# Kernel tuning notes

Hardware: AMD Instinct MI355X
Metric: run time of the kernel (lower is better)

## Reference

```python
import jax, jax.numpy as jnp
import numpy as np

B_, T_, N_ = 32, 96, 68
IN_F, HID, GRU_H, NCLS = 3, 128, 128, 10
DEG = 8
N_NODES = B_ * T_ * N_
N_EDGES = N_NODES * DEG


def setup_inputs() -> dict:
    key = jax.random.key(0)
    ks = jax.random.split(key, 16)
    s = 0.05
    rn = lambda k, shp: (jax.random.normal(k, shp, jnp.float32) * s)
    return {
        "x": jax.random.normal(ks[0], (N_NODES, IN_F), jnp.float32),
        "edge_index": jax.random.randint(ks[1], (2, N_EDGES), 0, N_NODES, jnp.int32),
        "W_gcn0": rn(ks[2], (IN_F, HID)),
        "b_gcn0": jnp.zeros((HID,), jnp.float32),
        "W_gcn1": rn(ks[3], (HID, HID)),
        "b_gcn1": jnp.zeros((HID,), jnp.float32),
        "W_mlp": rn(ks[4], (HID, HID)),
        "b_mlp": jnp.zeros((HID,), jnp.float32),
        "W_ih": rn(ks[5], (3 * GRU_H, HID)),
        "W_hh": rn(ks[6], (3 * GRU_H, GRU_H)),
        "b_ih": jnp.zeros((3 * GRU_H,), jnp.float32),
        "b_hh": jnp.zeros((3 * GRU_H,), jnp.float32),
        "W_c1": rn(ks[7], (GRU_H, GRU_H // 2)),
        "b_c1": jnp.zeros((GRU_H // 2,), jnp.float32),
        "W_c2": rn(ks[8], (GRU_H // 2, NCLS)),
        "b_c2": jnp.zeros((NCLS,), jnp.float32),
        "B": B_, "T": T_, "N": N_,
    }


def reference(x, edge_index, W_gcn0, b_gcn0, W_gcn1, b_gcn1, W_mlp, b_mlp,
              W_ih, W_hh, b_ih, b_hh, W_c1, b_c1, W_c2, b_c2, B, T, N):
    n_nodes = x.shape[0]
    src, dst = edge_index[0], edge_index[1]
    # GCN degree with self-loops: deg[i] = 1 + in-degree(i)
    deg = jnp.ones((n_nodes,), x.dtype).at[dst].add(1.0)
    d_isqrt = jax.lax.rsqrt(deg)
    self_norm = (d_isqrt * d_isqrt)[:, None]  # self-loop norm = 1/deg
    edge_norm = (d_isqrt[src] * d_isqrt[dst])[:, None]

    def gcn(h, W, b):
        h = h @ W
        agg = jax.ops.segment_sum(h[src] * edge_norm, dst, num_segments=n_nodes)
        return agg + h * self_norm + b

    h = jax.nn.relu(gcn(x, W_gcn0, b_gcn0))
    h = jax.nn.relu(gcn(h, W_gcn1, b_gcn1))
    h = jax.nn.relu(h @ W_mlp + b_mlp)  # node_mlp (dropout off in eval)

    frames = h.reshape(B, T, N, -1).mean(axis=2)  # [B, T, HID] frame pooling

    def gru_step(hs, xt):
        gi = xt @ W_ih.T + b_ih
        gh = hs @ W_hh.T + b_hh
        ir, iz, inn = jnp.split(gi, 3, axis=-1)
        hr, hz, hn = jnp.split(gh, 3, axis=-1)
        r = jax.nn.sigmoid(ir + hr)
        z = jax.nn.sigmoid(iz + hz)
        n_new = jnp.tanh(inn + r * hn)
        return (1.0 - z) * n_new + z * hs, None

    h0 = jnp.zeros((B, GRU_H), frames.dtype)
    hT, _ = jax.lax.scan(gru_step, h0, jnp.swapaxes(frames, 0, 1))

    hidden = jax.nn.relu(hT @ W_c1 + b_c1)
    return hidden @ W_c2 + b_c2  # logits [B, num_classes]
```

## Files before the change

### kernel.cpp

```cpp
#include <hip/hip_runtime.h>

#define NN_TOT 208896
#define E_TOT  1671168
#define B_SZ   32
#define T_SZ   96
#define NPF    68
#define HID    128
#define NBINS  204
#define CAP    9216
#define NSB    816

typedef _Float16 f16x8 __attribute__((ext_vector_type(8)));
typedef _Float16 f16x2v __attribute__((ext_vector_type(2)));
typedef float f32x4 __attribute__((ext_vector_type(4)));

__global__ __launch_bounds__(256) void k_scatter(const int* __restrict__ src, const int* __restrict__ dst,
                                                 int* __restrict__ gcur, int* __restrict__ er_tmp,
                                                 const float* __restrict__ Wih, const float* __restrict__ Whh,
                                                 const float* __restrict__ W1, const float* __restrict__ Wm,
                                                 const float* __restrict__ W0, const float* __restrict__ b0,
                                                 _Float16* __restrict__ Wihh, _Float16* __restrict__ Wihl,
                                                 _Float16* __restrict__ W1p, _Float16* __restrict__ Wmp,
                                                 _Float16* __restrict__ Whhp, _Float16* __restrict__ W0h,
                                                 _Float16* __restrict__ b0h) {
    const int bid = blockIdx.x;
    const int tid = threadIdx.x;
    if (bid >= NSB) {
        int i = (bid - NSB) * 256 + tid;
        {
            int e = i & 7;
            int lane = (i >> 3) & 63;
            int f = i >> 9;
            int j = f >> 2, kk = f & 3;
            int q = lane >> 4, p = lane & 15;
            float wv = Wih[(size_t)(j * 16 + p) * 128 + kk * 32 + q * 8 + e];
            _Float16 hi = (_Float16)wv;
            Wihh[i] = hi;
            Wihl[i] = (_Float16)(wv - (float)hi);
        }
        {
            int e = i & 7;
            int lane = (i >> 3) & 63;
            int f = i >> 9;
            int kk = f & 3, g = (f >> 2) % 3, wv = f / 12;
            int q = lane >> 4, c = lane & 15;
            Whhp[i] = (_Float16)Whh[(size_t)(g * 128 + 16 * wv + c) * 128 + kk * 32 + q * 8 + e];
        }
        if (i < 16384) {
            int f = i >> 9;
            int j = f >> 2, kk = f & 3;
            int lane = (i >> 3) & 63;
            int e = i & 7;
            int q = lane >> 4, p = lane & 15;
            int k = kk * 32 + q * 8 + e, n = j * 16 + p;
            W1p[i] = (_Float16)W1[k * 128 + n];
            Wmp[i] = (_Float16)Wm[k * 128 + n];
        }
        if (i < 384) W0h[i] = (_Float16)W0[i];
        if (i < 128) b0h[i] = (_Float16)b0[i];
        return;
    }
    __shared__ int hist[NBINS];
    __shared__ int lofs[NBINS];
    __shared__ int lbase[NBINS];
    __shared__ int ts[256];
    __shared__ int recs[2048];
    __shared__ int dsta[2048];
    for (int i = tid; i < NBINS; i += 256) hist[i] = 0;
    __syncthreads();
    const int be = bid * 2048 + tid * 8;
    int s[8], d[8], rk[8];
    *(int4*)&s[0] = *(const int4*)&src[be];
    *(int4*)&s[4] = *(const int4*)&src[be + 4];
    *(int4*)&d[0] = *(const int4*)&dst[be];
    *(int4*)&d[4] = *(const int4*)&dst[be + 4];
#pragma unroll
    for (int j = 0; j < 8; ++j) rk[j] = atomicAdd(&hist[d[j] >> 10], 1);
    __syncthreads();
    {
        int v = (tid < NBINS) ? hist[tid] : 0;
        ts[tid] = v;
        __syncthreads();
        int inc = v;
        for (int off = 1; off < 256; off <<= 1) {
            int add = (tid >= off) ? ts[tid - off] : 0;
            __syncthreads();
            inc += add;
            ts[tid] = inc;
            __syncthreads();
        }
        if (tid < NBINS) lofs[tid] = inc - v;
    }
    for (int i = tid; i < NBINS; i += 256) lbase[i] = atomicAdd(&gcur[i], hist[i]);
    __syncthreads();
#pragma unroll
    for (int j = 0; j < 8; ++j) {
        int b = d[j] >> 10;
        int pos = lofs[b] + rk[j];
        recs[pos] = s[j] | ((d[j] & 1023) << 18);
        dsta[pos] = b * CAP + lbase[b] + rk[j];
    }
    __syncthreads();
#pragma unroll
    for (int it = 0; it < 8; ++it) {
        int p = tid + it * 256;
        er_tmp[dsta[p]] = recs[p];
    }
}

__global__ __launch_bounds__(256) void k_binsort2(const int* __restrict__ er_tmp, const int* __restrict__ gcur,
                                                  const float* __restrict__ x, int* __restrict__ er,
                                                  int2* __restrict__ row2, float4* __restrict__ xd) {
    __shared__ int lcnt[1024];
    __shared__ int lofs[1024];
    __shared__ int ts[256];
    const int tid = threadIdx.x;
    const int nb = blockIdx.x << 10;
    const int base0 = blockIdx.x * CAP;
    for (int i = tid; i < 1024; i += 256) lcnt[i] = 0;
    __syncthreads();
    const int nrec = gcur[blockIdx.x];
    int rec[36];
#pragma unroll
    for (int j = 0; j < 36; ++j) {
        int idx = tid + j * 256;
        rec[j] = (idx < nrec) ? er_tmp[base0 + idx] : -1;
    }
#pragma unroll
    for (int j = 0; j < 36; ++j)
        if (rec[j] >= 0) atomicAdd(&lcnt[rec[j] >> 18], 1);
    __syncthreads();
    const int base = tid * 4;
    const int c0 = lcnt[base], c1 = lcnt[base + 1], c2 = lcnt[base + 2], c3 = lcnt[base + 3];
    int ssum = c0 + c1 + c2 + c3;
    ts[tid] = ssum;
    __syncthreads();
    int inc = ssum;
    for (int off = 1; off < 256; off <<= 1) {
        int add = (tid >= off) ? ts[tid - off] : 0;
        __syncthreads();
        inc += add;
        ts[tid] = inc;
        __syncthreads();
    }
    const int b0 = base0 + (inc - ssum);
    lofs[base] = b0;
    lofs[base + 1] = b0 + c0;
    lofs[base + 2] = b0 + c0 + c1;
    lofs[base + 3] = b0 + c0 + c1 + c2;
    row2[nb + base] = make_int2(b0, b0 + c0);
    row2[nb + base + 1] = make_int2(b0 + c0, b0 + c0 + c1);
    row2[nb + base + 2] = make_int2(b0 + c0 + c1, b0 + c0 + c1 + c2);
    row2[nb + base + 3] = make_int2(b0 + c0 + c1 + c2, b0 + ssum);
    {
        const float4* xv = (const float4*)(x + 3 * (size_t)(nb + base));
        float4 a = xv[0], b = xv[1], c = xv[2];
        float i0 = 1.0f / sqrtf(1.f + (float)c0);
        float i1 = 1.0f / sqrtf(1.f + (float)c1);
        float i2 = 1.0f / sqrtf(1.f + (float)c2);
        float i3 = 1.0f / sqrtf(1.f + (float)c3);
        xd[nb + base + 0] = make_float4(a.x * i0, a.y * i0, a.z * i0, i0);
        xd[nb + base + 1] = make_float4(a.w * i1, b.x * i1, b.y * i1, i1);
        xd[nb + base + 2] = make_float4(b.z * i2, b.w * i2, c.x * i2, i2);
        xd[nb + base + 3] = make_float4(c.y * i3, c.z * i3, c.w * i3, i3);
    }
    __syncthreads();
#pragma unroll
    for (int j = 0; j < 36; ++j)
        if (rec[j] >= 0) {
            int p = atomicAdd(&lofs[rec[j] >> 18], 1);
            er[p] = rec[j] & 0x3FFFF;
        }
}

__global__ __launch_bounds__(256) void k_z0(const float4* __restrict__ xd, const int2* __restrict__ row2,
                                            const int* __restrict__ er, float4* __restrict__ z0out) {
    const int tid = threadIdx.x;
    const int blk = blockIdx.x;
    const int li = tid >> 2;
    const int slot = tid & 3;
    const int n = blk * 64 + li;
    const int2 be2 = row2[n];
    float p0 = 0.f, p1 = 0.f, p2 = 0.f;
    for (int ei = be2.x + slot; ei < be2.y; ei += 4) {
        float4 f = xd[er[ei]];
        p0 += f.x;
        p1 += f.y;
        p2 += f.z;
    }
    p0 += __shfl_xor(p0, 1); p1 += __shfl_xor(p1, 1); p2 += __shfl_xor(p2, 1);
    p0 += __shfl_xor(p0, 2); p1 += __shfl_xor(p1, 2); p2 += __shfl_xor(p2, 2);
    if (slot == 0) {
        const float4 own = xd[n];
        const float w = own.w;
        float4 z;
        z.x = w * (p0 + own.x);
        z.y = w * (p1 + own.y);
        z.z = w * (p2 + own.z);
        z.w = w;
        z0out[n] = z;
    }
}

__global__ __launch_bounds__(256, 4) void k_agg_mm(const float4* __restrict__ z0, const int2* __restrict__ row2,
                                                   const int* __restrict__ er, const _Float16* __restrict__ W0h,
                                                   const _Float16* __restrict__ b0h, const _Float16* __restrict__ W1p,
                                                   const float* __restrict__ b1, const _Float16* __restrict__ Wmp,
                                                   const float* __restrict__ bm, float* __restrict__ fr32, int bofs) {
    __shared__ __align__(16) _Float16 As[64 * 136];
    __shared__ __align__(16) _Float16 Bs[64 * 136];
    __shared__ float colpart[4 * 2 * 128];
    const int tid = threadIdx.x;
    const int w = tid >> 6, lane = tid & 63;
    const int blk = blockIdx.x + bofs;

    {
        const int node = blk * 64 + lane;
        const int2 be2 = row2[node];
        const int beg = be2.x, end = be2.y;
        int ei = beg;
        int sa_c = 0, sb_c = 0, sa_n = 0, sb_n = 0;
        float4 za_c, zb_c;
        if (ei + 2 <= end) { sa_c = er[ei]; sb_c = er[ei + 1]; }
        if (ei + 4 <= end) { sa_n = er[ei + 2]; sb_n = er[ei + 3]; }
        const float4 zs = z0[node];
        if (ei + 2 <= end) { za_c = z0[sa_c]; zb_c = z0[sb_c]; }

        const f16x2v* __restrict__ W0p = (const f16x2v*)W0h;
        const f16x2v* __restrict__ b0p = (const f16x2v*)b0h;
        const int pb = w * 16;
        const f16x2v zero2 = {(_Float16)0.f, (_Float16)0.f};
        f16x2v w0p[16], w1p[16], w2p[16], bbp[16];
#pragma unroll
        for (int j = 0; j < 16; ++j) {
            w0p[j] = W0p[pb + j];
            w1p[j] = W0p[64 + pb + j];
            w2p[j] = W0p[128 + pb + j];
            bbp[j] = b0p[pb + j];
        }
        const _Float16 isd = (_Float16)zs.w;
        const f16x2v dnn = {isd, isd};
        f16x2v accp[16];
        {
            _Float16 sx = (_Float16)zs.x, sy = (_Float16)zs.y, sz = (_Float16)zs.z;
            f16x2v zxx = {sx, sx}, zyy = {sy, sy}, zzz = {sz, sz};
#pragma unroll
            for (int j = 0; j < 16; ++j) {
                f16x2v t = zxx * w0p[j] + (zyy * w1p[j] + (zzz * w2p[j] + bbp[j]));
                t = __builtin_elementwise_max(t, zero2);
                accp[j] = t * dnn;
            }
        }
        for (; ei + 2 <= end; ei += 2) {
            float4 za_nv, zb_nv;
            int sa_nn = 0, sb_nn = 0;
            if (ei + 4 <= end) { za_nv = z0[sa_n]; zb_nv = z0[sb_n]; }
            if (ei + 6 <= end) { sa_nn = er[ei + 4]; sb_nn = er[ei + 5]; }
            const float4 za = za_c, zb = zb_c;
            _Float16 ax = (_Float16)za.x, ay = (_Float16)za.y, az = (_Float16)za.z;
            _Float16 aen = (_Float16)za.w;
            _Float16 bx = (_Float16)zb.x, by = (_Float16)zb.y, bz = (_Float16)zb.z;
            _Float16 ben = (_Float16)zb.w;
            f16x2v axx = {ax, ax}, ayy = {ay, ay}, azz = {az, az}, aee = {aen, aen};
            f16x2v bxx = {bx, bx}, byy = {by, by}, bzz = {bz, bz}, bee = {ben, ben};
#pragma unroll
            for (int j = 0; j < 16; ++j) {
                f16x2v t = axx * w0p[j] + (ayy * w1p[j] + (azz * w2p[j] + bbp[j]));
                t = __builtin_elementwise_max(t, zero2);
                accp[j] = t * aee + accp[j];
            }
#pragma unroll
            for (int j = 0; j < 16; ++j) {
                f16x2v t = bxx * w0p[j] + (byy * w1p[j] + (bzz * w2p[j] + bbp[j]));
                t = __builtin_elementwise_max(t, zero2);
                accp[j] = t * bee + accp[j];
            }
            za_c = za_nv; zb_c = zb_nv;
            sa_n = sa_nn; sb_n = sb_nn;
        }
        if (ei < end) {
            float4 za = z0[er[ei]];
            _Float16 ax = (_Float16)za.x, ay = (_Float16)za.y, az = (_Float16)za.z;
            _Float16 aen = (_Float16)za.w;
            f16x2v axx = {ax, ax}, ayy = {ay, ay}, azz = {az, az}, aee = {aen, aen};
#pragma unroll
            for (int j = 0; j < 16; ++j) {
                f16x2v t = axx * w0p[j] + (ayy * w1p[j] + (azz * w2p[j] + bbp[j]));
                t = __builtin_elementwise_max(t, zero2);
                accp[j] = t * aee + accp[j];
            }
        }
        _Float16* dst = &As[lane * 136 + w * 32];
#pragma unroll
        for (int j = 0; j < 16; ++j) *(f16x2v*)(dst + 2 * j) = accp[j] * dnn;
    }
    __syncthreads();

    const int q = lane >> 4, c = lane & 15;
    {
        f16x8 afr[4];
#pragma unroll
        for (int kk = 0; kk < 4; ++kk) afr[kk] = *(const f16x8*)(&As[(w * 16 + c) * 136 + kk * 32 + q * 8]);
        const f16x8* __restrict__ Bv = (const f16x8*)W1p;
#pragma unroll
        for (int j = 0; j < 8; ++j) {
            f32x4 cc = {0.f, 0.f, 0.f, 0.f};
#pragma unroll
            for (int kk = 0; kk < 4; ++kk)
                cc = __builtin_amdgcn_mfma_f32_16x16x32_f16(afr[kk], Bv[(j * 4 + kk) * 64 + lane], cc, 0, 0, 0);
            const float bi = b1[j * 16 + c];
#pragma unroll
            for (int r = 0; r < 4; ++r)
                Bs[(w * 16 + q * 4 + r) * 136 + j * 16 + c] = (_Float16)fmaxf(cc[r] + bi, 0.f);
        }
    }

    {
        f16x8 afr2[4];
#pragma unroll
        for (int kk = 0; kk < 4; ++kk) afr2[kk] = *(const f16x8*)(&Bs[(w * 16 + c) * 136 + kk * 32 + q * 8]);
        const f16x8* __restrict__ Bv2 = (const f16x8*)Wmp;
        const int f0 = (blk * 64) / NPF;
        const int cut = (f0 + 1) * NPF;
        const int rowg0 = blk * 64 + w * 16 + q * 4;
#pragma unroll
        for (int j = 0; j < 8; ++j) {
            f32x4 cc = {0.f, 0.f, 0.f, 0.f};
#pragma unroll
            for (int kk = 0; kk < 4; ++kk)
                cc = __builtin_amdgcn_mfma_f32_16x16x32_f16(afr2[kk], Bv2[(j * 4 + kk) * 64 + lane], cc, 0, 0, 0);
            const float bi = bm[j * 16 + c];
            float sA = 0.f, sB = 0.f;
#pragma unroll
            for (int r = 0; r < 4; ++r) {
                float v = fmaxf(cc[r] + bi, 0.f);
                if (rowg0 + r < cut) sA += v; else sB += v;
            }
            sA += __shfl_xor(sA, 16);
            sA += __shfl_xor(sA, 32);
            sB += __shfl_xor(sB, 16);
            sB += __shfl_xor(sB, 32);
            if (lane < 16) {
                colpart[(w * 2 + 0) * 128 + j * 16 + c] = sA;
                colpart[(w * 2 + 1) * 128 + j * 16 + c] = sB;
            }
        }
    }
    __syncthreads();
    {
        const int f = tid >> 7, col = tid & 127;
        float s = colpart[(0 * 2 + f) * 128 + col] + colpart[(1 * 2 + f) * 128 + col] +
                  colpart[(2 * 2 + f) * 128 + col] + colpart[(3 * 2 + f) * 128 + col];
        const int f0 = (blk * 64) / NPF;
        if (f == 0) {
            atomicAdd(&fr32[(size_t)f0 * 128 + col], s);
        } else {
            const int f1 = (blk * 64 + 63) / NPF;
            if (f1 != f0) atomicAdd(&fr32[(size_t)f1 * 128 + col], s);
        }
    }
}

__global__ __launch_bounds__(256) void k_gi(const float* __restrict__ fr32,
                                            const _Float16* __restrict__ Wihh, const _Float16* __restrict__ Wihl,
                                            const float* __restrict__ bih, const float* __restrict__ bhh,
                                            float* __restrict__ GIt) {
    __shared__ __align__(16) _Float16 Ah[64 * 136];
    __shared__ __align__(16) _Float16 Al[64 * 136];
    const int tid = threadIdx.x;
    const int w = tid >> 6, lane = tid & 63;
    const int q = lane >> 4, p = lane & 15;
    const int nb = blockIdx.x * 64;

    for (int idx = tid; idx < 64 * 128; idx += 256) {
        int row = idx >> 7, col = idx & 127;
        float v = fr32[(size_t)(nb + row) * 128 + col] * (1.0f / NPF);
        _Float16 hi = (_Float16)v;
        Ah[row * 136 + col] = hi;
        Al[row * 136 + col] = (_Float16)(v - (float)hi);
    }
    __syncthreads();

    f16x8 ah[4], al[4];
#pragma unroll
    for (int kk = 0; kk < 4; ++kk) {
        ah[kk] = *(const f16x8*)(&Ah[(w * 16 + p) * 136 + kk * 32 + q * 8]);
        al[kk] = *(const f16x8*)(&Al[(w * 16 + p) * 136 + kk * 32 + q * 8]);
    }
    const f16x8* __restrict__ Bh = (const f16x8*)Wihh;
    const f16x8* __restrict__ Bl = (const f16x8*)Wihl;
    int dr[4];
#pragma unroll
    for (int r = 0; r < 4; ++r) {
        int m = nb + w * 16 + q * 4 + r;
        int bb = m / 96, tt = m - bb * 96;
        dr[r] = (tt * B_SZ + bb) * 384;
    }
#pragma unroll
    for (int j = 0; j < 24; ++j) {
        f32x4 cc = {0.f, 0.f, 0.f, 0.f};
#pragma unroll
        for (int kk = 0; kk < 4; ++kk)
            cc = __builtin_amdgcn_mfma_f32_16x16x32_f16(ah[kk], Bh[(j * 4 + kk) * 64 + lane], cc, 0, 0, 0);
#pragma unroll
        for (int kk = 0; kk < 4; ++kk)
            cc = __builtin_amdgcn_mfma_f32_16x16x32_f16(ah[kk], Bl[(j * 4 + kk) * 64 + lane], cc, 0, 0, 0);
#pragma unroll
        for (int kk = 0; kk < 4; ++kk)
            cc = __builtin_amdgcn_mfma_f32_16x16x32_f16(al[kk], Bh[(j * 4 + kk) * 64 + lane], cc, 0, 0, 0);
        const int o = j * 16 + p;
        const float bias = bih[o] + ((o < 256) ? bhh[o] : 0.f);
        const float scale = (o < 256) ? -1.44269504f : 1.f;
#pragma unroll
        for (int r = 0; r < 4; ++r) GIt[dr[r] + o] = (cc[r] + bias) * scale;
    }
}

#define GRU_SYNC()                                              \
    asm volatile("s_waitcnt lgkmcnt(0)" ::: "memory");          \
    __builtin_amdgcn_s_barrier();                               \
    __builtin_amdgcn_sched_barrier(0);

#define GRU_BODY(PAR, GU, GL, JOFF)                                                                  \
    {                                                                                                \
        const _Float16* rb = hbuf[PAR];                                                              \
        _Float16* wb = hbuf[PAR ^ 1];                                                                \
        f16x8 afr[4];                                                                                \
        _Pragma("unroll") for (int kk = 0; kk < 4; ++kk)                                             \
            afr[kk] = *(const f16x8*)(&rb[c * 144 + kk * 32 + q * 8]);                               \
        const float* lp = pb + (size_t)(JOFF + 2) * STRIDE;                                          \
        _Pragma("unroll") for (int r = 0; r < 4; ++r)                                                \
            _Pragma("unroll") for (int g = 0; g < 3; ++g)                                            \
                GL[r * 3 + g] = lp[r * 384 + g * 128];                                               \
        f32x4 cc[3];                                                                                 \
        _Pragma("unroll") for (int g = 0; g < 3; ++g) {                                              \
            f32x4 a = {0.f, 0.f, 0.f, 0.f};                                                          \
            _Pragma("unroll") for (int kk = 0; kk < 4; ++kk)                                         \
                a = __builtin_amdgcn_mfma_f32_16x16x32_f16(afr[kk], bfr[g][kk], a, 0, 0, 0);         \
            cc[g] = a;                                                                               \
        }                                                                                            \
        _Pragma("unroll") for (int r = 0; r < 4; ++r) {                                              \
            float hn = cc[2][r] + bh2;                                                               \
            float rg = __builtin_amdgcn_rcpf(1.f + exp2f(fmaf(mL2E, cc[0][r], GU[r * 3 + 0])));      \
            float zg = __builtin_amdgcn_rcpf(1.f + exp2f(fmaf(mL2E, cc[1][r], GU[r * 3 + 1])));      \
            float arg = fmaf(rg, hn, GU[r * 3 + 2]);                                                 \
            float u = __builtin_amdgcn_rcpf(exp2f(2.f * L2E * arg) + 1.f);                           \
            float nn = fmaf(-2.f, u, 1.f);                                                           \
            h[r] = fmaf(zg, h[r] - nn, nn);                                                          \
            if (q < 2) wb[(q * 4 + r) * 144 + 16 * w + c] = (_Float16)h[r];                          \
        }                                                                                            \
        GRU_SYNC()                                                                                   \
    }

__global__ __launch_bounds__(512) __attribute__((amdgpu_waves_per_eu(1, 2)))
void k_gru(const float* __restrict__ GIt, const _Float16* __restrict__ Whhp,
           const float* __restrict__ bhh,
           const float* __restrict__ Wc1, const float* __restrict__ bc1,
           const float* __restrict__ Wc2, const float* __restrict__ bc2,
           float* __restrict__ out, float* __restrict__ hst,
           int t0, int iters, int last) {
    __shared__ __align__(16) _Float16 hbuf[2][16 * 144];
    const int tid = threadIdx.x;
    const int w = tid >> 6, lane = tid & 63;
    const int q = lane >> 4, c = lane & 15;
    const int B = blockIdx.x;
    const float L2E = 1.44269504f;
    const float mL2E = -1.44269504f;
    const int STRIDE = B_SZ * 384;

    f16x8 bfr[3][4];
#pragma unroll
    for (int g = 0; g < 3; ++g)
#pragma unroll
        for (int kk = 0; kk < 4; ++kk)
            bfr[g][kk] = *(const f16x8*)(Whhp + (size_t)(((w * 3 + g) * 4 + kk) * 64 + lane) * 8);
    const float bh2 = bhh[256 + 16 * w + c];
    for (int i = tid; i < 2 * 16 * 144 / 2; i += 512) ((unsigned int*)hbuf)[i] = 0u;
    float h[4] = {0.f, 0.f, 0.f, 0.f};

    const int qq = (q < 2) ? q : 1;
    if (t0 != 0) {
#pragma unroll
        for (int r = 0; r < 4; ++r) h[r] = hst[(size_t)(B * 8 + qq * 4 + r) * 128 + 16 * w + c];
    }
    const float* pb = GIt + (size_t)t0 * STRIDE + (size_t)(B * 8 + qq * 4) * 384 + 16 * w + c;
    float g0[12], g1[12], g2[12];
#pragma unroll
    for (int r = 0; r < 4; ++r)
#pragma unroll
        for (int g = 0; g < 3; ++g) {
            g0[r * 3 + g] = pb[r * 384 + g * 128];
            g1[r * 3 + g] = pb[STRIDE + r * 384 + g * 128];
        }
    __syncthreads();
    if (t0 != 0 && q < 2) {
#pragma unroll
        for (int r = 0; r < 4; ++r) hbuf[0][(q * 4 + r) * 144 + 16 * w + c] = (_Float16)h[r];
    }
    GRU_SYNC()

    for (int it = 0; it < iters; ++it) {
        GRU_BODY(0, g0, g2, 0)
        GRU_BODY(1, g1, g0, 1)
        GRU_BODY(0, g2, g1, 2)
        GRU_BODY(1, g0, g2, 3)
        GRU_BODY(0, g1, g0, 4)
        GRU_BODY(1, g2, g1, 5)
        pb += 6 * (size_t)STRIDE;
    }

    if (!last) {
        if (q < 2) {
#pragma unroll
            for (int r = 0; r < 4; ++r) hst[(size_t)(B * 8 + q * 4 + r) * 128 + 16 * w + c] = h[r];
        }
        return;
    }

    float* hbf = (float*)hbuf;
    float* hid = hbf + 1024;
    __syncthreads();
    if (q < 2) {
#pragma unroll
        for (int r = 0; r < 4; ++r) hbf[(q * 4 + r) * 128 + 16 * w + c] = h[r];
    }
    __syncthreads();
    {
        const int b = tid >> 6, j = tid & 63;
        const float* hb = hbf + b * 128;
        float a0 = bc1[j], a1 = 0.f, a2 = 0.f, a3 = 0.f;
#pragma unroll
        for (int k = 0; k < 128; k += 4) {
            a0 = fmaf(hb[k], Wc1[k * 64 + j], a0);
            a1 = fmaf(hb[k + 1], Wc1[(k + 1) * 64 + j], a1);
            a2 = fmaf(hb[k + 2], Wc1[(k + 2) * 64 + j], a2);
            a3 = fmaf(hb[k + 3], Wc1[(k + 3) * 64 + j], a3);
        }
        hid[tid] = fmaxf((a0 + a1) + (a2 + a3), 0.f);
    }
    __syncthreads();
    if (tid < 80) {
        int b = tid / 10, cc2 = tid % 10;
        float a = bc2[cc2];
#pragma unroll 8
        for (int k = 0; k < 64; ++k) a = fmaf(hid[b * 64 + k], Wc2[k * 10 + cc2], a);
        out[(B * 8 + b) * 10 + cc2] = a;
    }
}

extern "C" void kernel_launch(void* const* d_in, const int* in_sizes, int n_in, void* d_out, int out_size, void* d_ws,
                              size_t ws_size, hipStream_t stream) {
    const float* x = (const float*)d_in[0];
    const int* ei = (const int*)d_in[1];
    const int* e_src = ei;
    const int* e_dst = ei + E_TOT;
    const float* W0 = (const float*)d_in[2];
    const float* b0 = (const float*)d_in[3];
    const float* W1 = (const float*)d_in[4];
    const float* b1 = (const float*)d_in[5];
    const float* Wm = (const float*)d_in[6];
    const float* bm = (const float*)d_in[7];
    const float* Wih = (const float*)d_in[8];
    const float* Whh = (const float*)d_in[9];
    const float* bih = (const float*)d_in[10];
    const float* bhh = (const float*)d_in[11];
    const float* Wc1 = (const float*)d_in[12];
    const float* bc1 = (const float*)d_in[13];
    const float* Wc2 = (const float*)d_in[14];
    const float* bc2 = (const float*)d_in[15];
    float* out = (float*)d_out;

    char* base = (char*)d_ws;
    size_t off = 0;
    auto alloc = [&](size_t bytes) {
        size_t o = off;
        off = (off + bytes + 255) & ~(size_t)255;
        return o;
    };
    size_t o_gcur = alloc(256 * 4);
    size_t o_row2 = alloc((size_t)NN_TOT * 8);
    size_t o_er = alloc((size_t)NBINS * CAP * 4);
    size_t o_ertmp = alloc((size_t)NBINS * CAP * 4);
    size_t o_xd = alloc((size_t)NN_TOT * 16);
    size_t o_fr32 = alloc((size_t)B_SZ * T_SZ * 128 * 4);
    size_t o_gi = alloc((size_t)(T_SZ + 2) * B_SZ * 384 * 4);
    size_t o_hst = alloc((size_t)B_SZ * 128 * 4);
    size_t o_wihh = alloc((size_t)384 * 128 * 2);
    size_t o_wihl = alloc((size_t)384 * 128 * 2);
    size_t o_w1p = alloc((size_t)128 * 128 * 2);
    size_t o_wmp = alloc((size_t)128 * 128 * 2);
    size_t o_whhp = alloc((size_t)128 * 384 * 2);
    size_t o_w0h = alloc((size_t)384 * 2);
    size_t o_b0h = alloc((size_t)128 * 2);
    size_t o_z0 = alloc((size_t)NN_TOT * 16);
    if (off > ws_size) return;

    int* gcur = (int*)(base + o_gcur);
    int2* row2 = (int2*)(base + o_row2);
    int* er = (int*)(base + o_er);
    int* er_tmp = (int*)(base + o_ertmp);
    float4* xd = (float4*)(base + o_xd);
    float* fr32 = (float*)(base + o_fr32);
    float* GIt = (float*)(base + o_gi);
    float* hst = (float*)(base + o_hst);
    _Float16* Wihh = (_Float16*)(base + o_wihh);
    _Float16* Wihl = (_Float16*)(base + o_wihl);
    _Float16* W1p = (_Float16*)(base + o_w1p);
    _Float16* Wmp = (_Float16*)(base + o_wmp);
    _Float16* Whhp = (_Float16*)(base + o_whhp);
    _Float16* W0h = (_Float16*)(base + o_w0h);
    _Float16* b0h = (_Float16*)(base + o_b0h);
    float4* z0 = (float4*)(base + o_z0);

    hipMemsetAsync(base + o_gcur, 0, 256 * 4, stream);
    hipMemsetAsync(base + o_fr32, 0, (size_t)B_SZ * T_SZ * 128 * 4, stream);

    k_scatter<<<NSB + 192, 256, 0, stream>>>(e_src, e_dst, gcur, er_tmp,
                                             Wih, Whh, W1, Wm, W0, b0,
                                             Wihh, Wihl, W1p, Wmp, Whhp, W0h, b0h);
    k_binsort2<<<NBINS, 256, 0, stream>>>(er_tmp, gcur, x, er, row2, xd);
    k_z0<<<NN_TOT / 64, 256, 0, stream>>>(xd, row2, er, z0);
    k_agg_mm<<<1088, 256, 0, stream>>>(z0, row2, er, W0h, b0h, W1p, b1, Wmp, bm, fr32, 0);
    k_agg_mm<<<1088, 256, 0, stream>>>(z0, row2, er, W0h, b0h, W1p, b1, Wmp, bm, fr32, 1088);
    k_agg_mm<<<1088, 256, 0, stream>>>(z0, row2, er, W0h, b0h, W1p, b1, Wmp, bm, fr32, 2176);
    k_gi<<<B_SZ * T_SZ / 64, 256, 0, stream>>>(fr32, Wihh, Wihl, bih, bhh, GIt);
    k_gru<<<4, 512, 0, stream>>>(GIt, Whhp, bhh, Wc1, bc1, Wc2, bc2, out, hst, 0, 5, 0);
    k_gru<<<4, 512, 0, stream>>>(GIt, Whhp, bhh, Wc1, bc1, Wc2, bc2, out, hst, 30, 5, 0);
    k_gru<<<4, 512, 0, stream>>>(GIt, Whhp, bhh, Wc1, bc1, Wc2, bc2, out, hst, 60, 6, 1);
}
```

Measured before the change: 370.0 us.

## Merge split kernel launches, fold fr32 memset into scatter, precompute bin ranks

```diff
diff --git a/kernel.cpp b/kernel.cpp
--- a/kernel.cpp
+++ b/kernel.cpp
@@ -22,11 +22,16 @@
                                                  _Float16* __restrict__ Wihh, _Float16* __restrict__ Wihl,
                                                  _Float16* __restrict__ W1p, _Float16* __restrict__ Wmp,
                                                  _Float16* __restrict__ Whhp, _Float16* __restrict__ W0h,
-                                                 _Float16* __restrict__ b0h) {
+                                                 _Float16* __restrict__ b0h, float4* __restrict__ fr32v) {
     const int bid = blockIdx.x;
     const int tid = threadIdx.x;
     if (bid >= NSB) {
         int i = (bid - NSB) * 256 + tid;
+        {
+            const float4 z4 = make_float4(0.f, 0.f, 0.f, 0.f);
+            fr32v[(size_t)i * 2] = z4;
+            fr32v[(size_t)i * 2 + 1] = z4;
+        }
         {
             int e = i & 7;
             int lane = (i >> 3) & 63;
@@ -121,6 +126,7 @@
     __syncthreads();
     const int nrec = gcur[blockIdx.x];
     int rec[36];
+    int rnk[36];
 #pragma unroll
     for (int j = 0; j < 36; ++j) {
         int idx = tid + j * 256;
@@ -128,7 +134,7 @@
     }
 #pragma unroll
     for (int j = 0; j < 36; ++j)
-        if (rec[j] >= 0) atomicAdd(&lcnt[rec[j] >> 18], 1);
+        rnk[j] = (rec[j] >= 0) ? atomicAdd(&lcnt[rec[j] >> 18], 1) : 0;
     __syncthreads();
     const int base = tid * 4;
     const int c0 = lcnt[base], c1 = lcnt[base + 1], c2 = lcnt[base + 2], c3 = lcnt[base + 3];
@@ -167,10 +173,7 @@
     __syncthreads();
 #pragma unroll
     for (int j = 0; j < 36; ++j)
-        if (rec[j] >= 0) {
-            int p = atomicAdd(&lofs[rec[j] >> 18], 1);
-            er[p] = rec[j] & 0x3FFFF;
-        }
+        if (rec[j] >= 0) er[lofs[rec[j] >> 18] + rnk[j]] = rec[j] & 0x3FFFF;
 }
 
 __global__ __launch_bounds__(256) void k_z0(const float4* __restrict__ xd, const int2* __restrict__ row2,
@@ -206,13 +209,13 @@
                                                    const int* __restrict__ er, const _Float16* __restrict__ W0h,
                                                    const _Float16* __restrict__ b0h, const _Float16* __restrict__ W1p,
                                                    const float* __restrict__ b1, const _Float16* __restrict__ Wmp,
-                                                   const float* __restrict__ bm, float* __restrict__ fr32, int bofs) {
+                                                   const float* __restrict__ bm, float* __restrict__ fr32) {
     __shared__ __align__(16) _Float16 As[64 * 136];
     __shared__ __align__(16) _Float16 Bs[64 * 136];
     __shared__ float colpart[4 * 2 * 128];
     const int tid = threadIdx.x;
     const int w = tid >> 6, lane = tid & 63;
-    const int blk = blockIdx.x + bofs;
+    const int blk = blockIdx.x;
 
     {
         const int node = blk * 64 + lane;
@@ -457,8 +460,7 @@
            const float* __restrict__ bhh,
            const float* __restrict__ Wc1, const float* __restrict__ bc1,
            const float* __restrict__ Wc2, const float* __restrict__ bc2,
-           float* __restrict__ out, float* __restrict__ hst,
-           int t0, int iters, int last) {
+           float* __restrict__ out) {
     __shared__ __align__(16) _Float16 hbuf[2][16 * 144];
     const int tid = threadIdx.x;
     const int w = tid >> 6, lane = tid & 63;
@@ -479,11 +481,7 @@
     float h[4] = {0.f, 0.f, 0.f, 0.f};
 
     const int qq = (q < 2) ? q : 1;
-    if (t0 != 0) {
-#pragma unroll
-        for (int r = 0; r < 4; ++r) h[r] = hst[(size_t)(B * 8 + qq * 4 + r) * 128 + 16 * w + c];
-    }
-    const float* pb = GIt + (size_t)t0 * STRIDE + (size_t)(B * 8 + qq * 4) * 384 + 16 * w + c;
+    const float* pb = GIt + (size_t)(B * 8 + qq * 4) * 384 + 16 * w + c;
     float g0[12], g1[12], g2[12];
 #pragma unroll
     for (int r = 0; r < 4; ++r)
@@ -492,14 +490,9 @@
             g0[r * 3 + g] = pb[r * 384 + g * 128];
             g1[r * 3 + g] = pb[STRIDE + r * 384 + g * 128];
         }
-    __syncthreads();
-    if (t0 != 0 && q < 2) {
-#pragma unroll
-        for (int r = 0; r < 4; ++r) hbuf[0][(q * 4 + r) * 144 + 16 * w + c] = (_Float16)h[r];
-    }
     GRU_SYNC()
 
-    for (int it = 0; it < iters; ++it) {
+    for (int it = 0; it < T_SZ / 6; ++it) {
         GRU_BODY(0, g0, g2, 0)
         GRU_BODY(1, g1, g0, 1)
         GRU_BODY(0, g2, g1, 2)
@@ -507,14 +500,6 @@
         GRU_BODY(0, g1, g0, 4)
         GRU_BODY(1, g2, g1, 5)
         pb += 6 * (size_t)STRIDE;
-    }
-
-    if (!last) {
-        if (q < 2) {
-#pragma unroll
-            for (int r = 0; r < 4; ++r) hst[(size_t)(B * 8 + q * 4 + r) * 128 + 16 * w + c] = h[r];
-        }
-        return;
     }
 
     float* hbf = (float*)hbuf;
@@ -584,7 +569,6 @@
     size_t o_xd = alloc((size_t)NN_TOT * 16);
     size_t o_fr32 = alloc((size_t)B_SZ * T_SZ * 128 * 4);
     size_t o_gi = alloc((size_t)(T_SZ + 2) * B_SZ * 384 * 4);
-    size_t o_hst = alloc((size_t)B_SZ * 128 * 4);
     size_t o_wihh = alloc((size_t)384 * 128 * 2);
     size_t o_wihl = alloc((size_t)384 * 128 * 2);
     size_t o_w1p = alloc((size_t)128 * 128 * 2);
@@ -602,7 +586,6 @@
     float4* xd = (float4*)(base + o_xd);
     float* fr32 = (float*)(base + o_fr32);
     float* GIt = (float*)(base + o_gi);
-    float* hst = (float*)(base + o_hst);
     _Float16* Wihh = (_Float16*)(base + o_wihh);
     _Float16* Wihl = (_Float16*)(base + o_wihl);
     _Float16* W1p = (_Float16*)(base + o_w1p);
@@ -613,18 +596,13 @@
     float4* z0 = (float4*)(base + o_z0);
 
     hipMemsetAsync(base + o_gcur, 0, 256 * 4, stream);
-    hipMemsetAsync(base + o_fr32, 0, (size_t)B_SZ * T_SZ * 128 * 4, stream);
 
     k_scatter<<<NSB + 192, 256, 0, stream>>>(e_src, e_dst, gcur, er_tmp,
                                              Wih, Whh, W1, Wm, W0, b0,
-                                             Wihh, Wihl, W1p, Wmp, Whhp, W0h, b0h);
+                                             Wihh, Wihl, W1p, Wmp, Whhp, W0h, b0h, (float4*)fr32);
     k_binsort2<<<NBINS, 256, 0, stream>>>(er_tmp, gcur, x, er, row2, xd);
     k_z0<<<NN_TOT / 64, 256, 0, stream>>>(xd, row2, er, z0);
-    k_agg_mm<<<1088, 256, 0, stream>>>(z0, row2, er, W0h, b0h, W1p, b1, Wmp, bm, fr32, 0);
-    k_agg_mm<<<1088, 256, 0, stream>>>(z0, row2, er, W0h, b0h, W1p, b1, Wmp, bm, fr32, 1088);
-    k_agg_mm<<<1088, 256, 0, stream>>>(z0, row2, er, W0h, b0h, W1p, b1, Wmp, bm, fr32, 2176);
+    k_agg_mm<<<NN_TOT / 64, 256, 0, stream>>>(z0, row2, er, W0h, b0h, W1p, b1, Wmp, bm, fr32);
     k_gi<<<B_SZ * T_SZ / 64, 256, 0, stream>>>(fr32, Wihh, Wihl, bih, bhh, GIt);
-    k_gru<<<4, 512, 0, stream>>>(GIt, Whhp, bhh, Wc1, bc1, Wc2, bc2, out, hst, 0, 5, 0);
-    k_gru<<<4, 512, 0, stream>>>(GIt, Whhp, bhh, Wc1, bc1, Wc2, bc2, out, hst, 30, 5, 0);
-    k_gru<<<4, 512, 0, stream>>>(GIt, Whhp, bhh, Wc1, bc1, Wc2, bc2, out, hst, 60, 6, 1);
+    k_gru<<<4, 512, 0, stream>>>(GIt, Whhp, bhh, Wc1, bc1, Wc2, bc2, out);
 }
```

Result: faster. 338.3 us (-8.6%).
